# Performance work log

Hardware: AMD Instinct MI355X
Metric: run time of the kernel (lower is better)

## Reference

```python
import jax, jax.numpy as jnp
import numpy as np

B, I, H, O = 32768, 256, 512, 128
STEPS = 10
SPARSITY = 0.8
LN_EPS = 1e-5


def _layernorm(x, g, b):
    mu = jnp.mean(x, axis=-1, keepdims=True)
    var = jnp.mean(jnp.square(x - mu), axis=-1, keepdims=True)
    return (x - mu) * jax.lax.rsqrt(var + LN_EPS) * g + b


def _liquid_layer(x_in, W_in, W_rec, bias, tau, A, mask, g, b):
    """One LiquidLayer: STEPS semi-implicit ODE steps + per-step LayerNorm."""
    dt = 1.0 / STEPS
    i_input = x_in @ W_in                      # [B, H], constant across steps
    Wr_T = (W_rec * mask).T                    # sparse recurrent weights, [H, H]

    def step(h, _):
        f = jax.nn.sigmoid(i_input + h @ Wr_T + bias)
        h_new = (h + dt * f * A) / (1.0 + dt / tau + dt * f)
        return _layernorm(h_new, g, b), None

    h0 = jnp.zeros_like(i_input)
    h, _ = jax.lax.scan(step, h0, None, length=STEPS)
    return h


def setup_inputs() -> dict:
    key = jax.random.key(0)
    ks = jax.random.split(key, 16)
    inp = {
        "x": jax.random.normal(ks[0], (B, I), jnp.float32),
        "W_in_0": jax.random.normal(ks[1], (I, H), jnp.float32) * 0.1,
        "W_rec_0": jax.random.normal(ks[2], (H, H), jnp.float32) * 0.1,
        "bias_0": jnp.zeros((H,), jnp.float32),
        "tau_0": jnp.ones((H,), jnp.float32),
        "A_0": jnp.ones((H,), jnp.float32),
        "mask_0": (jax.random.uniform(ks[3], (H, H)) > SPARSITY).astype(jnp.float32),
        "ln_g_0": jnp.ones((H,), jnp.float32),
        "ln_b_0": jnp.zeros((H,), jnp.float32),
        "W_in_1": jax.random.normal(ks[4], (H, H), jnp.float32) * 0.1,
        "W_rec_1": jax.random.normal(ks[5], (H, H), jnp.float32) * 0.1,
        "bias_1": jnp.zeros((H,), jnp.float32),
        "tau_1": jnp.ones((H,), jnp.float32),
        "A_1": jnp.ones((H,), jnp.float32),
        "mask_1": (jax.random.uniform(ks[6], (H, H)) > SPARSITY).astype(jnp.float32),
        "ln_g_1": jnp.ones((H,), jnp.float32),
        "ln_b_1": jnp.zeros((H,), jnp.float32),
        "W_in_2": jax.random.normal(ks[7], (H, H), jnp.float32) * 0.1,
        "W_rec_2": jax.random.normal(ks[8], (H, H), jnp.float32) * 0.1,
        "bias_2": jnp.zeros((H,), jnp.float32),
        "tau_2": jnp.ones((H,), jnp.float32),
        "A_2": jnp.ones((H,), jnp.float32),
        "mask_2": (jax.random.uniform(ks[9], (H, H)) > SPARSITY).astype(jnp.float32),
        "ln_g_2": jnp.ones((H,), jnp.float32),
        "ln_b_2": jnp.zeros((H,), jnp.float32),
        "out_W": jax.random.normal(ks[10], (O, H), jnp.float32) * (1.0 / np.sqrt(H)),
        "out_b": jnp.zeros((O,), jnp.float32),
    }
    return inp


def reference(x,
              W_in_0, W_rec_0, bias_0, tau_0, A_0, mask_0, ln_g_0, ln_b_0,
              W_in_1, W_rec_1, bias_1, tau_1, A_1, mask_1, ln_g_1, ln_b_1,
              W_in_2, W_rec_2, bias_2, tau_2, A_2, mask_2, ln_g_2, ln_b_2,
              out_W, out_b):
    h = _liquid_layer(x, W_in_0, W_rec_0, bias_0, tau_0, A_0, mask_0, ln_g_0, ln_b_0)
    h = _liquid_layer(h, W_in_1, W_rec_1, bias_1, tau_1, A_1, mask_1, ln_g_1, ln_b_1)
    h = _liquid_layer(h, W_in_2, W_rec_2, bias_2, tau_2, A_2, mask_2, ln_g_2, ln_b_2)
    return h @ out_W.T + out_b  # output projection of the final (output) layer
```

## Files before the change

kernel.cpp:

```cpp
#include <hip/hip_runtime.h>

#define HDIM   512
#define BROWS  64
#define LDA    520
#define NSTEPS 10
#define DT     0.1f
#define LNEPS  1e-5f

typedef __attribute__((ext_vector_type(8))) short v8s;
typedef __attribute__((ext_vector_type(4))) float v4f;

static __device__ __forceinline__ ushort f2bf(float f) {
  union { float f; unsigned u; } v; v.f = f;
  unsigned r = v.u + 0x7fffu + ((v.u >> 16) & 1u);
  return (ushort)(r >> 16);
}
static __device__ __forceinline__ float bf2f(unsigned hw) {
  union { unsigned u; float f; } v; v.u = hw << 16;
  return v.f;
}

__global__ void pack_w(const float* __restrict__ src, const float* __restrict__ msk,
                       ushort* __restrict__ dst, int K, int N, int trans) {
  int nt = N >> 4;
  int tot = (K >> 5) * nt * 64;
  int f = blockIdx.x * blockDim.x + threadIdx.x;
  if (f >= tot) return;
  int flane = f & 63;
  int rest = f >> 6;
  int ctg = rest % nt;
  int kc = rest / nt;
  int n = ctg * 16 + (flane & 15);
  int kb = kc * 32 + ((flane >> 4) & 3) * 8;
  ushort v[8];
#pragma unroll
  for (int j = 0; j < 8; ++j) {
    int k = kb + j;
    float s;
    if (trans) {
      s = src[(size_t)n * K + k];
      if (msk) s *= msk[(size_t)n * K + k];
    } else {
      s = src[(size_t)k * N + n];
    }
    v[j] = f2bf(s);
  }
  uint4 u;
  u.x = (unsigned)v[0] | ((unsigned)v[1] << 16);
  u.y = (unsigned)v[2] | ((unsigned)v[3] << 16);
  u.z = (unsigned)v[4] | ((unsigned)v[5] << 16);
  u.w = (unsigned)v[6] | ((unsigned)v[7] << 16);
  *(uint4*)(dst + (size_t)f * 8) = u;
}

template <int KC, int NT, int NCT>
static __device__ __forceinline__ void gemm_tiles(const ushort* hb, const ushort* __restrict__ w,
                                                  int wv, int lane, v4f acc[4][4]) {
  const int q = lane >> 4, n = lane & 15;
#pragma unroll
  for (int rt = 0; rt < 4; ++rt)
#pragma unroll
    for (int ct = 0; ct < NCT; ++ct)
      acc[rt][ct] = (v4f){0.f, 0.f, 0.f, 0.f};
#pragma unroll
  for (int kc = 0; kc < KC; ++kc) {
    v8s a[4];
#pragma unroll
    for (int rt = 0; rt < 4; ++rt)
      a[rt] = *(const v8s*)(hb + (rt * 16 + n) * LDA + kc * 32 + q * 8);
#pragma unroll
    for (int ct = 0; ct < NCT; ++ct) {
      const int ctg = wv * NCT + ct;
      v8s b = *(const v8s*)(w + ((size_t)(kc * NT + ctg) * 64 + lane) * 8);
#pragma unroll
      for (int rt = 0; rt < 4; ++rt)
        acc[rt][ct] = __builtin_amdgcn_mfma_f32_16x16x32_bf16(a[rt], b, acc[rt][ct], 0, 0, 0);
    }
  }
}

struct LayerP {
  const ushort* win;
  const ushort* wrec;
  const float* bias;
  const float* tau;
  const float* Aamp;
  const float* g;
  const float* b;
};
struct KP {
  const float* x;
  LayerP L[3];
  const ushort* wout;
  const float* outb;
  float* out;
};

__global__ __launch_bounds__(512, 2) void liquid_fused(KP P) {
  extern __shared__ char smem[];
  ushort* hb = (ushort*)smem;
  float2* stats = (float2*)(smem + BROWS * LDA * 2);
  float2* stats2 = stats + BROWS * 8;

  const int tid = threadIdx.x;
  const int wv = tid >> 6;
  const int lane = tid & 63;
  const int q = lane >> 4;
  const int n = lane & 15;
  const int row0 = blockIdx.x * BROWS;
  const int wc0 = wv * 64;

  {
    const float4* x4 = (const float4*)P.x;
#pragma unroll
    for (int i = 0; i < 8; ++i) {
      int fi = i * 512 + tid;
      int r = fi >> 6;
      int c4 = fi & 63;
      float4 v = x4[(size_t)(row0 + r) * 64 + c4];
      uint2 o;
      o.x = (unsigned)f2bf(v.x) | ((unsigned)f2bf(v.y) << 16);
      o.y = (unsigned)f2bf(v.z) | ((unsigned)f2bf(v.w) << 16);
      *(uint2*)(hb + r * LDA + c4 * 4) = o;
    }
  }
  __syncthreads();

  v4f acc[4][4];
  v4f base[4][4];
  unsigned hsp[4][4][2];
  float ac[4], c1[4], gc[4], bc[4];

#pragma unroll 1
  for (int l = 0; l < 3; ++l) {
    const LayerP& L = P.L[l];
    float biasc[4];
#pragma unroll
    for (int ct = 0; ct < 4; ++ct) {
      int col = wc0 + ct * 16 + n;
      biasc[ct] = L.bias[col];
      ac[ct] = DT * L.Aamp[col];
      c1[ct] = 1.0f + DT / L.tau[col];
      gc[ct] = L.g[col];
      bc[ct] = L.b[col];
    }

    if (l == 0) gemm_tiles<8, 32, 4>(hb, L.win, wv, lane, acc);
    else        gemm_tiles<16, 32, 4>(hb, L.win, wv, lane, acc);
#pragma unroll
    for (int rt = 0; rt < 4; ++rt)
#pragma unroll
      for (int ct = 0; ct < 4; ++ct) {
        base[rt][ct][0] = acc[rt][ct][0] + biasc[ct];
        base[rt][ct][1] = acc[rt][ct][1] + biasc[ct];
        base[rt][ct][2] = acc[rt][ct][2] + biasc[ct];
        base[rt][ct][3] = acc[rt][ct][3] + biasc[ct];
      }

#pragma unroll 1
    for (int s = 0; s < NSTEPS; ++s) {
      if (s > 0) {
        gemm_tiles<16, 32, 4>(hb, L.wrec, wv, lane, acc);
      } else {
#pragma unroll
        for (int rt = 0; rt < 4; ++rt)
#pragma unroll
          for (int ct = 0; ct < 4; ++ct)
            acc[rt][ct] = (v4f){0.f, 0.f, 0.f, 0.f};
      }

#pragma unroll
      for (int rt = 0; rt < 4; ++rt)
#pragma unroll
        for (int ct = 0; ct < 4; ++ct)
#pragma unroll
          for (int r = 0; r < 4; ++r) {
            float arg = acc[rt][ct][r] + base[rt][ct][r];
            float fv = __builtin_amdgcn_rcpf(1.0f + __expf(-arg));
            float hold = (s == 0) ? 0.0f
                                  : bf2f((hsp[rt][ct][r >> 1] >> ((r & 1) * 16)) & 0xffffu);
            acc[rt][ct][r] = (hold + fv * ac[ct]) *
                             __builtin_amdgcn_rcpf(c1[ct] + DT * fv);
          }

      float ps[4][4], p2[4][4];
#pragma unroll
      for (int rt = 0; rt < 4; ++rt)
#pragma unroll
        for (int r = 0; r < 4; ++r) {
          float sv = 0.f, s2 = 0.f;
#pragma unroll
          for (int ct = 0; ct < 4; ++ct) {
            float v = acc[rt][ct][r];
            sv += v;
            s2 = fmaf(v, v, s2);
          }
          ps[rt][r] = sv;
          p2[rt][r] = s2;
        }
#pragma unroll
      for (int m = 1; m <= 8; m <<= 1)
#pragma unroll
        for (int rt = 0; rt < 4; ++rt)
#pragma unroll
          for (int r = 0; r < 4; ++r) {
            ps[rt][r] += __shfl_xor(ps[rt][r], m);
            p2[rt][r] += __shfl_xor(p2[rt][r], m);
          }
      if (n == 0) {
#pragma unroll
        for (int rt = 0; rt < 4; ++rt)
#pragma unroll
          for (int r = 0; r < 4; ++r)
            stats[(rt * 16 + q * 4 + r) * 8 + wv] = make_float2(ps[rt][r], p2[rt][r]);
      }
      __syncthreads();
      if (tid < BROWS) {
        float S = 0.f, S2 = 0.f;
#pragma unroll
        for (int i = 0; i < 8; ++i) {
          float2 t = stats[tid * 8 + i];
          S += t.x;
          S2 += t.y;
        }
        float mu = S * (1.0f / HDIM);
        float var = fmaf(-mu, mu, S2 * (1.0f / HDIM));
        stats2[tid] = make_float2(mu, __builtin_amdgcn_rsqf(var + LNEPS));
      }
      __syncthreads();

      float2 stv[4][4];
#pragma unroll
      for (int rt = 0; rt < 4; ++rt)
#pragma unroll
        for (int r = 0; r < 4; ++r)
          stv[rt][r] = stats2[rt * 16 + q * 4 + r];
#pragma unroll
      for (int rt = 0; rt < 4; ++rt) {
#pragma unroll
        for (int ct = 0; ct < 4; ++ct) {
          ushort hv[4];
#pragma unroll
          for (int r = 0; r < 4; ++r) {
            float v = (acc[rt][ct][r] - stv[rt][r].x) * stv[rt][r].y * gc[ct] + bc[ct];
            hv[r] = f2bf(v);
            hb[(rt * 16 + q * 4 + r) * LDA + wc0 + ct * 16 + n] = hv[r];
          }
          hsp[rt][ct][0] = (unsigned)hv[0] | ((unsigned)hv[1] << 16);
          hsp[rt][ct][1] = (unsigned)hv[2] | ((unsigned)hv[3] << 16);
        }
      }
      __syncthreads();
    }
  }

  v4f oa[4];
#pragma unroll
  for (int rt = 0; rt < 4; ++rt) oa[rt] = (v4f){0.f, 0.f, 0.f, 0.f};
#pragma unroll
  for (int kc = 0; kc < 16; ++kc) {
    v8s b = *(const v8s*)(P.wout + ((size_t)(kc * 8 + wv) * 64 + lane) * 8);
#pragma unroll
    for (int rt = 0; rt < 4; ++rt) {
      v8s a = *(const v8s*)(hb + (rt * 16 + n) * LDA + kc * 32 + q * 8);
      oa[rt] = __builtin_amdgcn_mfma_f32_16x16x32_bf16(a, b, oa[rt], 0, 0, 0);
    }
  }
  {
    int col = wv * 16 + n;
    float ob = P.outb[col];
#pragma unroll
    for (int rt = 0; rt < 4; ++rt)
#pragma unroll
      for (int r = 0; r < 4; ++r)
        P.out[(size_t)(row0 + rt * 16 + q * 4 + r) * 128 + col] = oa[rt][r] + ob;
  }
}

extern "C" void kernel_launch(void* const* d_in, const int* in_sizes, int n_in,
                              void* d_out, int out_size, void* d_ws, size_t ws_size,
                              hipStream_t stream) {
  (void)in_sizes; (void)n_in; (void)out_size; (void)ws_size;
  ushort* ws = (ushort*)d_ws;

  const size_t S_WIN0 = 0;
  const size_t S_WIN1 = S_WIN0 + (size_t)8 * 32 * 64 * 8;
  const size_t S_WIN2 = S_WIN1 + (size_t)16 * 32 * 64 * 8;
  const size_t S_REC0 = S_WIN2 + (size_t)16 * 32 * 64 * 8;
  const size_t S_REC1 = S_REC0 + (size_t)16 * 32 * 64 * 8;
  const size_t S_REC2 = S_REC1 + (size_t)16 * 32 * 64 * 8;
  const size_t S_WOUT = S_REC2 + (size_t)16 * 32 * 64 * 8;

  const float* f[27];
  for (int i = 0; i < 27; ++i) f[i] = (const float*)d_in[i];

  dim3 bt(256);
  pack_w<<<dim3(64),  bt, 0, stream>>>(f[1],  nullptr, ws + S_WIN0, 256, 512, 0);
  pack_w<<<dim3(128), bt, 0, stream>>>(f[9],  nullptr, ws + S_WIN1, 512, 512, 0);
  pack_w<<<dim3(128), bt, 0, stream>>>(f[17], nullptr, ws + S_WIN2, 512, 512, 0);
  pack_w<<<dim3(128), bt, 0, stream>>>(f[2],  f[6],    ws + S_REC0, 512, 512, 1);
  pack_w<<<dim3(128), bt, 0, stream>>>(f[10], f[14],   ws + S_REC1, 512, 512, 1);
  pack_w<<<dim3(128), bt, 0, stream>>>(f[18], f[22],   ws + S_REC2, 512, 512, 1);
  pack_w<<<dim3(32),  bt, 0, stream>>>(f[25], nullptr, ws + S_WOUT, 512, 128, 1);

  KP P;
  P.x = f[0];
  const size_t win_off[3] = {S_WIN0, S_WIN1, S_WIN2};
  const size_t rec_off[3] = {S_REC0, S_REC1, S_REC2};
  for (int l = 0; l < 3; ++l) {
    int bi = 1 + 8 * l;
    P.L[l].win = ws + win_off[l];
    P.L[l].wrec = ws + rec_off[l];
    P.L[l].bias = f[bi + 2];
    P.L[l].tau = f[bi + 3];
    P.L[l].Aamp = f[bi + 4];
    P.L[l].g = f[bi + 6];
    P.L[l].b = f[bi + 7];
  }
  P.wout = ws + S_WOUT;
  P.outb = f[26];
  P.out = (float*)d_out;

  const int smem = BROWS * LDA * 2 + BROWS * 8 * 8 + BROWS * 8;
  hipFuncSetAttribute((const void*)liquid_fused,
                      hipFuncAttributeMaxDynamicSharedMemorySize, smem);
  liquid_fused<<<dim3(32768 / BROWS), dim3(512), smem, stream>>>(P);
}
```

Baseline: 1.097 ms.

## Halve block rows to raise occupancy; use packed bf16 cvt and DPP row reductions

Shrinks each block's batch tile from 64 to 32 rows and raises launch bounds to four blocks per SM, cutting register and LDS use so more waves can hide latency. It also switches to the hardware packed bf16 conversion instruction, replaces shfl_xor reductions with DPP row-sum reductions, and fuses the layernorm sum accumulation into the ODE update loop. The trade-off is that each weight fragment is reused across fewer row tiles, so global and L2 weight traffic per MFMA doubles.

```diff
diff --git a/kernel.cpp b/kernel.cpp
--- a/kernel.cpp
+++ b/kernel.cpp
@@ -1,7 +1,7 @@
 #include <hip/hip_runtime.h>
 
 #define HDIM   512
-#define BROWS  64
+#define BROWS  32
 #define LDA    520
 #define NSTEPS 10
 #define DT     0.1f
@@ -18,6 +18,20 @@
 static __device__ __forceinline__ float bf2f(unsigned hw) {
   union { unsigned u; float f; } v; v.u = hw << 16;
   return v.f;
+}
+static __device__ __forceinline__ unsigned cvt_pk_bf16(float lo, float hi) {
+  unsigned r;
+  asm("v_cvt_pk_bf16_f32 %0, %1, %2" : "=v"(r) : "v"(lo), "v"(hi));
+  return r;
+}
+static __device__ __forceinline__ float rowsum16(float x) {
+  union { float f; int i; } u, v;
+  u.f = x;
+  v.i = __builtin_amdgcn_update_dpp(0, u.i, 0x121, 0xf, 0xf, false); u.f += v.f;
+  v.i = __builtin_amdgcn_update_dpp(0, u.i, 0x122, 0xf, 0xf, false); u.f += v.f;
+  v.i = __builtin_amdgcn_update_dpp(0, u.i, 0x124, 0xf, 0xf, false); u.f += v.f;
+  v.i = __builtin_amdgcn_update_dpp(0, u.i, 0x128, 0xf, 0xf, false); u.f += v.f;
+  return u.f;
 }
 
 __global__ void pack_w(const float* __restrict__ src, const float* __restrict__ msk,
@@ -53,27 +67,27 @@
   *(uint4*)(dst + (size_t)f * 8) = u;
 }
 
-template <int KC, int NT, int NCT>
+template <int KC, int NT, int NCT, int RT>
 static __device__ __forceinline__ void gemm_tiles(const ushort* hb, const ushort* __restrict__ w,
-                                                  int wv, int lane, v4f acc[4][4]) {
+                                                  int wv, int lane, v4f acc[RT][NCT]) {
   const int q = lane >> 4, n = lane & 15;
 #pragma unroll
-  for (int rt = 0; rt < 4; ++rt)
+  for (int rt = 0; rt < RT; ++rt)
 #pragma unroll
     for (int ct = 0; ct < NCT; ++ct)
       acc[rt][ct] = (v4f){0.f, 0.f, 0.f, 0.f};
 #pragma unroll
   for (int kc = 0; kc < KC; ++kc) {
-    v8s a[4];
-#pragma unroll
-    for (int rt = 0; rt < 4; ++rt)
+    v8s a[RT];
+#pragma unroll
+    for (int rt = 0; rt < RT; ++rt)
       a[rt] = *(const v8s*)(hb + (rt * 16 + n) * LDA + kc * 32 + q * 8);
 #pragma unroll
     for (int ct = 0; ct < NCT; ++ct) {
       const int ctg = wv * NCT + ct;
       v8s b = *(const v8s*)(w + ((size_t)(kc * NT + ctg) * 64 + lane) * 8);
 #pragma unroll
-      for (int rt = 0; rt < 4; ++rt)
+      for (int rt = 0; rt < RT; ++rt)
         acc[rt][ct] = __builtin_amdgcn_mfma_f32_16x16x32_bf16(a[rt], b, acc[rt][ct], 0, 0, 0);
     }
   }
@@ -96,7 +110,7 @@
   float* out;
 };
 
-__global__ __launch_bounds__(512, 2) void liquid_fused(KP P) {
+__global__ __launch_bounds__(512, 4) void liquid_fused(KP P) {
   extern __shared__ char smem[];
   ushort* hb = (ushort*)smem;
   float2* stats = (float2*)(smem + BROWS * LDA * 2);
@@ -113,64 +127,65 @@
   {
     const float4* x4 = (const float4*)P.x;
 #pragma unroll
-    for (int i = 0; i < 8; ++i) {
+    for (int i = 0; i < 4; ++i) {
       int fi = i * 512 + tid;
       int r = fi >> 6;
       int c4 = fi & 63;
       float4 v = x4[(size_t)(row0 + r) * 64 + c4];
       uint2 o;
-      o.x = (unsigned)f2bf(v.x) | ((unsigned)f2bf(v.y) << 16);
-      o.y = (unsigned)f2bf(v.z) | ((unsigned)f2bf(v.w) << 16);
+      o.x = cvt_pk_bf16(v.x, v.y);
+      o.y = cvt_pk_bf16(v.z, v.w);
       *(uint2*)(hb + r * LDA + c4 * 4) = o;
     }
   }
   __syncthreads();
 
-  v4f acc[4][4];
-  v4f base[4][4];
-  unsigned hsp[4][4][2];
+  v4f acc[2][4];
+  v4f base[2][4];
+  unsigned hsp[2][4][2];
   float ac[4], c1[4], gc[4], bc[4];
 
 #pragma unroll 1
   for (int l = 0; l < 3; ++l) {
     const LayerP& L = P.L[l];
-    float biasc[4];
 #pragma unroll
     for (int ct = 0; ct < 4; ++ct) {
       int col = wc0 + ct * 16 + n;
-      biasc[ct] = L.bias[col];
       ac[ct] = DT * L.Aamp[col];
       c1[ct] = 1.0f + DT / L.tau[col];
       gc[ct] = L.g[col];
       bc[ct] = L.b[col];
     }
 
-    if (l == 0) gemm_tiles<8, 32, 4>(hb, L.win, wv, lane, acc);
-    else        gemm_tiles<16, 32, 4>(hb, L.win, wv, lane, acc);
-#pragma unroll
-    for (int rt = 0; rt < 4; ++rt)
-#pragma unroll
-      for (int ct = 0; ct < 4; ++ct) {
-        base[rt][ct][0] = acc[rt][ct][0] + biasc[ct];
-        base[rt][ct][1] = acc[rt][ct][1] + biasc[ct];
-        base[rt][ct][2] = acc[rt][ct][2] + biasc[ct];
-        base[rt][ct][3] = acc[rt][ct][3] + biasc[ct];
-      }
+    if (l == 0) gemm_tiles<8, 32, 4, 2>(hb, L.win, wv, lane, acc);
+    else        gemm_tiles<16, 32, 4, 2>(hb, L.win, wv, lane, acc);
+#pragma unroll
+    for (int ct = 0; ct < 4; ++ct) {
+      float bias = L.bias[wc0 + ct * 16 + n];
+#pragma unroll
+      for (int rt = 0; rt < 2; ++rt)
+#pragma unroll
+        for (int r = 0; r < 4; ++r)
+          base[rt][ct][r] = acc[rt][ct][r] + bias;
+    }
 
 #pragma unroll 1
     for (int s = 0; s < NSTEPS; ++s) {
       if (s > 0) {
-        gemm_tiles<16, 32, 4>(hb, L.wrec, wv, lane, acc);
+        gemm_tiles<16, 32, 4, 2>(hb, L.wrec, wv, lane, acc);
       } else {
 #pragma unroll
-        for (int rt = 0; rt < 4; ++rt)
+        for (int rt = 0; rt < 2; ++rt)
 #pragma unroll
           for (int ct = 0; ct < 4; ++ct)
             acc[rt][ct] = (v4f){0.f, 0.f, 0.f, 0.f};
       }
 
 #pragma unroll
-      for (int rt = 0; rt < 4; ++rt)
+      for (int rt = 0; rt < 2; ++rt) {
+        float ps[4], p2[4];
+#pragma unroll
+        for (int r = 0; r < 4; ++r) { ps[r] = 0.f; p2[r] = 0.f; }
 #pragma unroll
         for (int ct = 0; ct < 4; ++ct)
 #pragma unroll
@@ -179,40 +194,18 @@
             float fv = __builtin_amdgcn_rcpf(1.0f + __expf(-arg));
             float hold = (s == 0) ? 0.0f
                                   : bf2f((hsp[rt][ct][r >> 1] >> ((r & 1) * 16)) & 0xffffu);
-            acc[rt][ct][r] = (hold + fv * ac[ct]) *
-                             __builtin_amdgcn_rcpf(c1[ct] + DT * fv);
+            float hn = (hold + fv * ac[ct]) * __builtin_amdgcn_rcpf(c1[ct] + DT * fv);
+            acc[rt][ct][r] = hn;
+            ps[r] += hn;
+            p2[r] = fmaf(hn, hn, p2[r]);
           }
-
-      float ps[4][4], p2[4][4];
-#pragma unroll
-      for (int rt = 0; rt < 4; ++rt)
-#pragma unroll
-        for (int r = 0; r < 4; ++r) {
-          float sv = 0.f, s2 = 0.f;
-#pragma unroll
-          for (int ct = 0; ct < 4; ++ct) {
-            float v = acc[rt][ct][r];
-            sv += v;
-            s2 = fmaf(v, v, s2);
-          }
-          ps[rt][r] = sv;
-          p2[rt][r] = s2;
+#pragma unroll
+        for (int r = 0; r < 4; ++r) { ps[r] = rowsum16(ps[r]); p2[r] = rowsum16(p2[r]); }
+        if (n == 0) {
+#pragma unroll
+          for (int r = 0; r < 4; ++r)
+            stats[(rt * 16 + q * 4 + r) * 8 + wv] = make_float2(ps[r], p2[r]);
         }
-#pragma unroll
-      for (int m = 1; m <= 8; m <<= 1)
-#pragma unroll
-        for (int rt = 0; rt < 4; ++rt)
-#pragma unroll
-          for (int r = 0; r < 4; ++r) {
-            ps[rt][r] += __shfl_xor(ps[rt][r], m);
-            p2[rt][r] += __shfl_xor(p2[rt][r], m);
-          }
-      if (n == 0) {
-#pragma unroll
-        for (int rt = 0; rt < 4; ++rt)
-#pragma unroll
-          for (int r = 0; r < 4; ++r)
-            stats[(rt * 16 + q * 4 + r) * 8 + wv] = make_float2(ps[rt][r], p2[rt][r]);
       }
       __syncthreads();
       if (tid < BROWS) {
@@ -229,39 +222,41 @@
       }
       __syncthreads();
 
-      float2 stv[4][4];
-#pragma unroll
-      for (int rt = 0; rt < 4; ++rt)
+#pragma unroll
+      for (int rt = 0; rt < 2; ++rt) {
+        float2 st[4];
 #pragma unroll
         for (int r = 0; r < 4; ++r)
-          stv[rt][r] = stats2[rt * 16 + q * 4 + r];
-#pragma unroll
-      for (int rt = 0; rt < 4; ++rt) {
+          st[r] = stats2[rt * 16 + q * 4 + r];
 #pragma unroll
         for (int ct = 0; ct < 4; ++ct) {
-          ushort hv[4];
-#pragma unroll
-          for (int r = 0; r < 4; ++r) {
-            float v = (acc[rt][ct][r] - stv[rt][r].x) * stv[rt][r].y * gc[ct] + bc[ct];
-            hv[r] = f2bf(v);
-            hb[(rt * 16 + q * 4 + r) * LDA + wc0 + ct * 16 + n] = hv[r];
-          }
-          hsp[rt][ct][0] = (unsigned)hv[0] | ((unsigned)hv[1] << 16);
-          hsp[rt][ct][1] = (unsigned)hv[2] | ((unsigned)hv[3] << 16);
+          float v0 = (acc[rt][ct][0] - st[0].x) * st[0].y * gc[ct] + bc[ct];
+          float v1 = (acc[rt][ct][1] - st[1].x) * st[1].y * gc[ct] + bc[ct];
+          float v2 = (acc[rt][ct][2] - st[2].x) * st[2].y * gc[ct] + bc[ct];
+          float v3 = (acc[rt][ct][3] - st[3].x) * st[3].y * gc[ct] + bc[ct];
+          unsigned p01 = cvt_pk_bf16(v0, v1);
+          unsigned p23 = cvt_pk_bf16(v2, v3);
+          hsp[rt][ct][0] = p01;
+          hsp[rt][ct][1] = p23;
+          ushort* wp = hb + (rt * 16 + q * 4) * LDA + wc0 + ct * 16 + n;
+          wp[0]       = (ushort)p01;
+          wp[LDA]     = (ushort)(p01 >> 16);
+          wp[2 * LDA] = (ushort)p23;
+          wp[3 * LDA] = (ushort)(p23 >> 16);
         }
       }
       __syncthreads();
     }
   }
 
-  v4f oa[4];
-#pragma unroll
-  for (int rt = 0; rt < 4; ++rt) oa[rt] = (v4f){0.f, 0.f, 0.f, 0.f};
+  v4f oa[2];
+#pragma unroll
+  for (int rt = 0; rt < 2; ++rt) oa[rt] = (v4f){0.f, 0.f, 0.f, 0.f};
 #pragma unroll
   for (int kc = 0; kc < 16; ++kc) {
     v8s b = *(const v8s*)(P.wout + ((size_t)(kc * 8 + wv) * 64 + lane) * 8);
 #pragma unroll
-    for (int rt = 0; rt < 4; ++rt) {
+    for (int rt = 0; rt < 2; ++rt) {
       v8s a = *(const v8s*)(hb + (rt * 16 + n) * LDA + kc * 32 + q * 8);
       oa[rt] = __builtin_amdgcn_mfma_f32_16x16x32_bf16(a, b, oa[rt], 0, 0, 0);
     }
@@ -270,7 +265,7 @@
     int col = wv * 16 + n;
     float ob = P.outb[col];
 #pragma unroll
-    for (int rt = 0; rt < 4; ++rt)
+    for (int rt = 0; rt < 2; ++rt)
 #pragma unroll
       for (int r = 0; r < 4; ++r)
         P.out[(size_t)(row0 + rt * 16 + q * 4 + r) * 128 + col] = oa[rt][r] + ob;
```

Result: faster. 915.8 us (-16.5%).
